# Optimization experiments

Hardware: AMD Instinct MI355X
Metric: run time of the kernel (lower is better)

## Reference

```python
import jax, jax.numpy as jnp
import numpy as np

N = 50000      # num nodes
E = 800000     # num edges
D = 64         # in_dim = hid_dim = out_dim
K = 8          # propagation hops (num_layers)
ALPHA = 0.6


def setup_inputs() -> dict:
    key = jax.random.key(0)
    ks = jax.random.split(key, 6)
    s = 1.0 / np.sqrt(D)
    return {
        "x": jax.random.normal(ks[0], (N, D), jnp.float32),
        "w_conv": jax.random.normal(ks[1], (D, D), jnp.float32) * s,
        "b_conv": jnp.zeros((D,), jnp.float32),
        "w1": jax.random.normal(ks[2], (D, D), jnp.float32) * s,
        "b1": jnp.zeros((D,), jnp.float32),
        "w2": jax.random.normal(ks[3], (D, D), jnp.float32) * s,
        "b2": jnp.zeros((D,), jnp.float32),
        "edge_index": jax.random.randint(ks[4], (2, E), 0, N, jnp.int64),
    }


def _gcn_norm(edge_index, num_nodes):
    # add self loops, symmetric normalization D^-1/2 (A+I) D^-1/2
    loop = jnp.arange(num_nodes, dtype=edge_index.dtype)
    src = jnp.concatenate([edge_index[0], loop])
    dst = jnp.concatenate([edge_index[1], loop])
    ones = jnp.ones(src.shape[0], jnp.float32)
    deg = jax.ops.segment_sum(ones, dst, num_segments=num_nodes)
    dinv = jnp.where(deg > 0, jax.lax.rsqrt(deg), 0.0)
    norm = dinv[src] * dinv[dst]  # [E+N]
    return src, dst, norm


def reference(x, w_conv, b_conv, w1, b1, w2, b2, edge_index):
    num_nodes = x.shape[0]
    src, dst, norm = _gcn_norm(edge_index, num_nodes)
    # SSGConv: h = alpha*x + (1-alpha)/K * sum_k A_hat^k x
    h = ALPHA * x
    xk = x
    coef = (1.0 - ALPHA) / K
    for _ in range(K):
        xk = jax.ops.segment_sum(norm[:, None] * xk[src], dst, num_segments=num_nodes)
        h = h + coef * xk
    h = h @ w_conv.T + b_conv        # SSGConv's internal Linear
    h = jax.nn.relu(h)               # F.relu(conv1(...))
    h = jax.nn.relu(h @ w1.T + b1)   # lin1 + relu (dropout p=0, eval)
    return h @ w2.T + b2             # lin2
```

## Files before the change

### kernel.cpp

```cpp
#include <hip/hip_runtime.h>

#define DD 64
#define ALPHA 0.6f
#define KHOPS 8
#define WP 72

typedef __attribute__((ext_vector_type(8))) short bf16x8;
typedef __attribute__((ext_vector_type(4))) float f32x4;

static __device__ __forceinline__ unsigned short f2bf(float f) {
    unsigned int u = __float_as_uint(f);
    unsigned int r = (u + 0x7FFFu + ((u >> 16) & 1u)) >> 16;
    return (unsigned short)r;
}
static __device__ __forceinline__ unsigned int pack2bf(float lo, float hi) {
    return (unsigned int)f2bf(lo) | ((unsigned int)f2bf(hi) << 16);
}

__global__ __launch_bounds__(256) void deg_count_kernel(const int* __restrict__ dst,
                                                        int* __restrict__ cnt, int e) {
    int i = blockIdx.x * blockDim.x + threadIdx.x;
    if (i < e) atomicAdd(&cnt[dst[i]], 1);
}

__global__ __launch_bounds__(256) void dinv_kernel(const int* __restrict__ cnt,
                                                   float2* __restrict__ dinvr, int n) {
    int i = blockIdx.x * blockDim.x + threadIdx.x;
    if (i < n) {
        float d = (float)(cnt[i] + 1);
        dinvr[i] = make_float2(rsqrtf(d), sqrtf(d));
    }
}

__global__ __launch_bounds__(256) void scan1_kernel(const int* __restrict__ cnt,
                                                    int* __restrict__ partials, int n) {
    int i = blockIdx.x * 256 + threadIdx.x;
    int v = (i < n) ? cnt[i] : 0;
    #pragma unroll
    for (int off = 1; off < 64; off <<= 1) v += __shfl_down(v, off, 64);
    __shared__ int ws[4];
    if ((threadIdx.x & 63) == 0) ws[threadIdx.x >> 6] = v;
    __syncthreads();
    if (threadIdx.x == 0) partials[blockIdx.x] = ws[0] + ws[1] + ws[2] + ws[3];
}

__global__ __launch_bounds__(1024) void scan2_kernel(int* __restrict__ partials, int nb) {
    __shared__ int s[1024];
    int t = threadIdx.x;
    int v = (t < nb) ? partials[t] : 0;
    s[t] = v;
    __syncthreads();
    for (int off = 1; off < 1024; off <<= 1) {
        int tmp = (t >= off) ? s[t - off] : 0;
        __syncthreads();
        s[t] += tmp;
        __syncthreads();
    }
    if (t < nb) partials[t] = s[t] - v;
}

__global__ __launch_bounds__(256) void scan3_kernel(const int* __restrict__ cnt,
                                                    const int* __restrict__ partials,
                                                    int* __restrict__ rowptr,
                                                    int* __restrict__ cursor, int n) {
    int t = threadIdx.x;
    int i = blockIdx.x * 256 + t;
    int v = (i < n) ? cnt[i] : 0;
    int lane = t & 63;
    int incl = v;
    #pragma unroll
    for (int off = 1; off < 64; off <<= 1) {
        int u = __shfl_up(incl, off, 64);
        if (lane >= off) incl += u;
    }
    __shared__ int wsum[4];
    if (lane == 63) wsum[t >> 6] = incl;
    __syncthreads();
    int woff = 0;
    for (int w = 0; w < (t >> 6); ++w) woff += wsum[w];
    int excl = incl - v + woff + partials[blockIdx.x];
    if (i < n) { rowptr[i] = excl; cursor[i] = excl; }
    if (i == n - 1) rowptr[n] = excl + v;
}

__global__ __launch_bounds__(256) void fill_kernel(const int* __restrict__ src,
                                                   const int* __restrict__ dst,
                                                   int* __restrict__ cursor,
                                                   int* __restrict__ esrc, int e) {
    int i = blockIdx.x * blockDim.x + threadIdx.x;
    if (i >= e) return;
    int s = src[i], d = dst[i];
    int pos = atomicAdd(&cursor[d], 1);
    __builtin_nontemporal_store(s, &esrc[pos]);
}

__global__ __launch_bounds__(256) void init_kernel(const float4* __restrict__ x,
                                                   const float2* __restrict__ dinvr,
                                                   float4* __restrict__ h,
                                                   ushort4* __restrict__ yb, int n4) {
    int i = blockIdx.x * blockDim.x + threadIdx.x;
    if (i >= n4) return;
    int row = i >> 4;
    float di = dinvr[row].x;
    float4 v = x[i];
    h[i] = make_float4(ALPHA * v.x, ALPHA * v.y, ALPHA * v.z, ALPHA * v.w);
    ushort4 b;
    b.x = f2bf(di * v.x); b.y = f2bf(di * v.y);
    b.z = f2bf(di * v.z); b.w = f2bf(di * v.w);
    yb[i] = b;
}

static __device__ __forceinline__ void add8(float* acc, uint4 v) {
    acc[0] += __uint_as_float(v.x << 16);
    acc[1] += __uint_as_float(v.x & 0xffff0000u);
    acc[2] += __uint_as_float(v.y << 16);
    acc[3] += __uint_as_float(v.y & 0xffff0000u);
    acc[4] += __uint_as_float(v.z << 16);
    acc[5] += __uint_as_float(v.z & 0xffff0000u);
    acc[6] += __uint_as_float(v.w << 16);
    acc[7] += __uint_as_float(v.w & 0xffff0000u);
}

template <int DO_H>
__global__ __launch_bounds__(256) void hop_kernel(const int* __restrict__ rowptr,
                                                  const int* __restrict__ esrc,
                                                  const float2* __restrict__ dinvr,
                                                  const unsigned short* __restrict__ yin,
                                                  unsigned short* __restrict__ yout,
                                                  float* __restrict__ h,
                                                  float coef, int n) {
    int wid = (blockIdx.x * blockDim.x + threadIdx.x) >> 6;
    if (wid >= n) return;
    int lane = threadIdx.x & 63;
    int g = lane >> 3;
    int s = lane & 7;
    int node = wid;

    int e0 = rowptr[node];
    int e1 = rowptr[node + 1];

    float acc[8] = {0.f, 0.f, 0.f, 0.f, 0.f, 0.f, 0.f, 0.f};
    float yprev[8];
    float2 dr;

    if (g == 0) {
        dr = dinvr[node];
        uint4 v = *(const uint4*)(yin + (size_t)node * 64 + s * 8);
        yprev[0] = __uint_as_float(v.x << 16);
        yprev[1] = __uint_as_float(v.x & 0xffff0000u);
        yprev[2] = __uint_as_float(v.y << 16);
        yprev[3] = __uint_as_float(v.y & 0xffff0000u);
        yprev[4] = __uint_as_float(v.z << 16);
        yprev[5] = __uint_as_float(v.z & 0xffff0000u);
        yprev[6] = __uint_as_float(v.w << 16);
        yprev[7] = __uint_as_float(v.w & 0xffff0000u);
        #pragma unroll
        for (int j = 0; j < 8; ++j) acc[j] = yprev[j];
    }

    int deg = e1 - e0;
    int niter = (deg + 7) >> 3;
    int i = 0;
    for (; i + 1 < niter; i += 2) {
        int eA = e0 + (i << 3) + g;
        int eB = eA + 8;
        int sA = esrc[eA];
        bool vB = eB < e1;
        int sB = esrc[vB ? eB : (e1 - 1)];
        uint4 va = *(const uint4*)(yin + (size_t)sA * 64 + s * 8);
        uint4 vb = *(const uint4*)(yin + (size_t)sB * 64 + s * 8);
        if (!vB) vb = make_uint4(0u, 0u, 0u, 0u);
        add8(acc, va);
        add8(acc, vb);
    }
    if (i < niter) {
        int eA = e0 + (i << 3) + g;
        bool vA = eA < e1;
        int sA = esrc[vA ? eA : (e1 - 1)];
        uint4 va = *(const uint4*)(yin + (size_t)sA * 64 + s * 8);
        if (!vA) va = make_uint4(0u, 0u, 0u, 0u);
        add8(acc, va);
    }

    #pragma unroll
    for (int off = 8; off < 64; off <<= 1) {
        #pragma unroll
        for (int j = 0; j < 8; ++j) acc[j] += __shfl_xor(acc[j], off, 64);
    }

    if (g == 0) {
        float di = dr.x;
        float d2 = di * di;
        uint4 o;
        o.x = pack2bf(d2 * acc[0], d2 * acc[1]);
        o.y = pack2bf(d2 * acc[2], d2 * acc[3]);
        o.z = pack2bf(d2 * acc[4], d2 * acc[5]);
        o.w = pack2bf(d2 * acc[6], d2 * acc[7]);
        *(uint4*)(yout + (size_t)node * 64 + s * 8) = o;
        if (DO_H) {
            float rd = dr.y;
            float* hp = h + (size_t)node * 64 + s * 8;
            float4 h0 = *(float4*)hp;
            float4 h1 = *(float4*)(hp + 4);
            h0.x += coef * (rd * yprev[0] + di * acc[0]);
            h0.y += coef * (rd * yprev[1] + di * acc[1]);
            h0.z += coef * (rd * yprev[2] + di * acc[2]);
            h0.w += coef * (rd * yprev[3] + di * acc[3]);
            h1.x += coef * (rd * yprev[4] + di * acc[4]);
            h1.y += coef * (rd * yprev[5] + di * acc[5]);
            h1.z += coef * (rd * yprev[6] + di * acc[6]);
            h1.w += coef * (rd * yprev[7] + di * acc[7]);
            *(float4*)hp = h0;
            *(float4*)(hp + 4) = h1;
        }
    }
}

__global__ __launch_bounds__(256) void mlp_mfma_kernel(const float* __restrict__ hin,
                                                       const float* __restrict__ wc,
                                                       const float* __restrict__ bc,
                                                       const float* __restrict__ w1,
                                                       const float* __restrict__ b1,
                                                       const float* __restrict__ w2,
                                                       const float* __restrict__ b2,
                                                       float* __restrict__ out, int n) {
    __shared__ unsigned short wlds[3][64][WP];
    __shared__ unsigned short xlds[64][WP];
    int t = threadIdx.x;

    const float* wm[3] = {wc, w1, w2};
    #pragma unroll
    for (int m = 0; m < 3; ++m) {
        const float4* w4 = (const float4*)wm[m];
        #pragma unroll
        for (int k = 0; k < 4; ++k) {
            int fid = t + k * 256;
            int j = fid >> 4, c4 = fid & 15;
            float4 v = w4[fid];
            *(uint2*)&wlds[m][j][c4 * 4] =
                make_uint2(pack2bf(v.x, v.y), pack2bf(v.z, v.w));
        }
    }

    int r0 = blockIdx.x * 64;
    const float4* h4 = (const float4*)hin;
    #pragma unroll
    for (int k = 0; k < 4; ++k) {
        int fid = t + k * 256;
        int r = fid >> 4, c4 = fid & 15;
        int gr = r0 + r;
        float4 v = (gr < n) ? h4[(size_t)gr * 16 + c4]
                            : make_float4(0.f, 0.f, 0.f, 0.f);
        *(uint2*)&xlds[r][c4 * 4] = make_uint2(pack2bf(v.x, v.y), pack2bf(v.z, v.w));
    }
    __syncthreads();

    int lane = t & 63;
    int wv = t >> 6;
    int rbase = wv * 16;
    int lr = lane & 15;
    int kg = lane >> 4;
    const float* bias[3] = {bc, b1, b2};

    #pragma unroll
    for (int m = 0; m < 3; ++m) {
        bf16x8 a0 = *(bf16x8*)&xlds[rbase + lr][kg * 8];
        bf16x8 a1 = *(bf16x8*)&xlds[rbase + lr][32 + kg * 8];
        #pragma unroll
        for (int ct = 0; ct < 4; ++ct) {
            bf16x8 bv0 = *(bf16x8*)&wlds[m][ct * 16 + lr][kg * 8];
            bf16x8 bv1 = *(bf16x8*)&wlds[m][ct * 16 + lr][32 + kg * 8];
            f32x4 acc = {0.f, 0.f, 0.f, 0.f};
            acc = __builtin_amdgcn_mfma_f32_16x16x32_bf16(a0, bv0, acc, 0, 0, 0);
            acc = __builtin_amdgcn_mfma_f32_16x16x32_bf16(a1, bv1, acc, 0, 0, 0);
            float bb = bias[m][ct * 16 + lr];
            if (m < 2) {
                #pragma unroll
                for (int rg = 0; rg < 4; ++rg) {
                    float v = fmaxf(acc[rg] + bb, 0.0f);
                    xlds[rbase + kg * 4 + rg][ct * 16 + lr] = f2bf(v);
                }
            } else {
                #pragma unroll
                for (int rg = 0; rg < 4; ++rg) {
                    int gr = r0 + rbase + kg * 4 + rg;
                    if (gr < n) out[(size_t)gr * 64 + ct * 16 + lr] = acc[rg] + bb;
                }
            }
        }
    }
}

extern "C" void kernel_launch(void* const* d_in, const int* in_sizes, int n_in,
                              void* d_out, int out_size, void* d_ws, size_t ws_size,
                              hipStream_t stream) {
    const float* x      = (const float*)d_in[0];
    const float* w_conv = (const float*)d_in[1];
    const float* b_conv = (const float*)d_in[2];
    const float* w1     = (const float*)d_in[3];
    const float* b1     = (const float*)d_in[4];
    const float* w2     = (const float*)d_in[5];
    const float* b2     = (const float*)d_in[6];
    const int*   ei     = (const int*)d_in[7];

    int n = in_sizes[0] / DD;
    int e = in_sizes[7] / 2;
    const int* src = ei;
    const int* dst = ei + e;

    char* wsb = (char*)d_ws;
    int*    cnt      = (int*)(wsb + 0);
    float2* dinvr    = (float2*)(wsb + 256 * 1024);
    int*    rowptr   = (int*)(wsb + 768 * 1024);
    int*    cursor   = (int*)(wsb + 1024 * 1024);
    int*    partials = (int*)(wsb + 1280 * 1024);
    int*    esrc     = (int*)(wsb + 1344 * 1024);
    unsigned short* yb0 = (unsigned short*)(wsb + 1344 * 1024 + (size_t)e * 4);
    unsigned short* yb1 = yb0 + (size_t)n * DD;
    float* h = (float*)d_out;

    const int B = 256;
    int n4 = n * (DD / 4);
    int nb = (n + 255) / 256;

    hipMemsetAsync(cnt, 0, (size_t)n * sizeof(int), stream);
    deg_count_kernel<<<(e + B - 1) / B, B, 0, stream>>>(dst, cnt, e);
    dinv_kernel<<<(n + B - 1) / B, B, 0, stream>>>(cnt, dinvr, n);
    scan1_kernel<<<nb, B, 0, stream>>>(cnt, partials, n);
    scan2_kernel<<<1, 1024, 0, stream>>>(partials, nb);
    scan3_kernel<<<nb, B, 0, stream>>>(cnt, partials, rowptr, cursor, n);
    fill_kernel<<<(e + B - 1) / B, B, 0, stream>>>(src, dst, cursor, esrc, e);

    init_kernel<<<(n4 + B - 1) / B, B, 0, stream>>>(
        (const float4*)x, dinvr, (float4*)h, (ushort4*)yb0, n4);

    float coef = (1.0f - ALPHA) / (float)KHOPS;
    int hblocks = (int)(((size_t)n * 64 + B - 1) / B);

    unsigned short* cur = yb0;
    unsigned short* nxt = yb1;
    for (int k = 1; k <= KHOPS; ++k) {
        if (k % 2 == 0)
            hop_kernel<1><<<hblocks, B, 0, stream>>>(rowptr, esrc, dinvr, cur, nxt, h,
                                                     coef, n);
        else
            hop_kernel<0><<<hblocks, B, 0, stream>>>(rowptr, esrc, dinvr, cur, nxt, h,
                                                     coef, n);
        unsigned short* tmp = cur; cur = nxt; nxt = tmp;
    }

    mlp_mfma_kernel<<<(n + 63) / 64, B, 0, stream>>>(h, w_conv, b_conv, w1, b1,
                                                     w2, b2, (float*)d_out, n);
}
```

Before: 305.6 us.

## Partition CSR fill by XCD destination range and unroll hop gather by four

```diff
diff --git a/kernel.cpp b/kernel.cpp
--- a/kernel.cpp
+++ b/kernel.cpp
@@ -83,15 +83,33 @@
     if (i == n - 1) rowptr[n] = excl + v;
 }
 
+#define FCHUNK 2048
 __global__ __launch_bounds__(256) void fill_kernel(const int* __restrict__ src,
                                                    const int* __restrict__ dst,
                                                    int* __restrict__ cursor,
-                                                   int* __restrict__ esrc, int e) {
-    int i = blockIdx.x * blockDim.x + threadIdx.x;
-    if (i >= e) return;
-    int s = src[i], d = dst[i];
-    int pos = atomicAdd(&cursor[d], 1);
-    __builtin_nontemporal_store(s, &esrc[pos]);
+                                                   int* __restrict__ esrc, int e, int n) {
+    int xcd = blockIdx.x & 7;
+    int chunk = blockIdx.x >> 3;
+    int lo = (int)(((long long)n * xcd) >> 3);
+    int hi = (int)(((long long)n * (xcd + 1)) >> 3);
+    int base = chunk * FCHUNK + threadIdx.x * 8;
+    if (base >= e) return;
+    int4 s0 = *(const int4*)(src + base);
+    int4 s1 = *(const int4*)(src + base + 4);
+    int4 d0 = *(const int4*)(dst + base);
+    int4 d1 = *(const int4*)(dst + base + 4);
+    int sv[8] = {s0.x, s0.y, s0.z, s0.w, s1.x, s1.y, s1.z, s1.w};
+    int dv[8] = {d0.x, d0.y, d0.z, d0.w, d1.x, d1.y, d1.z, d1.w};
+    #pragma unroll
+    for (int j = 0; j < 8; ++j) {
+        if (base + j < e) {
+            int d = dv[j];
+            if (d >= lo && d < hi) {
+                int pos = atomicAdd(&cursor[d], 1);
+                esrc[pos] = sv[j];
+            }
+        }
+    }
 }
 
 __global__ __launch_bounds__(256) void init_kernel(const float4* __restrict__ x,
@@ -160,26 +178,27 @@
 
     int deg = e1 - e0;
     int niter = (deg + 7) >> 3;
-    int i = 0;
-    for (; i + 1 < niter; i += 2) {
+    int clampe = e1 - 1;
+    for (int i = 0; i < niter; i += 4) {
         int eA = e0 + (i << 3) + g;
-        int eB = eA + 8;
-        int sA = esrc[eA];
-        bool vB = eB < e1;
-        int sB = esrc[vB ? eB : (e1 - 1)];
+        int eB = eA + 8, eC = eA + 16, eD = eA + 24;
+        bool vA = eA < e1, vB = eB < e1, vC = eC < e1, vD = eD < e1;
+        int sA = esrc[vA ? eA : clampe];
+        int sB = esrc[vB ? eB : clampe];
+        int sC = esrc[vC ? eC : clampe];
+        int sD = esrc[vD ? eD : clampe];
         uint4 va = *(const uint4*)(yin + (size_t)sA * 64 + s * 8);
         uint4 vb = *(const uint4*)(yin + (size_t)sB * 64 + s * 8);
+        uint4 vc = *(const uint4*)(yin + (size_t)sC * 64 + s * 8);
+        uint4 vd = *(const uint4*)(yin + (size_t)sD * 64 + s * 8);
+        if (!vA) va = make_uint4(0u, 0u, 0u, 0u);
         if (!vB) vb = make_uint4(0u, 0u, 0u, 0u);
+        if (!vC) vc = make_uint4(0u, 0u, 0u, 0u);
+        if (!vD) vd = make_uint4(0u, 0u, 0u, 0u);
         add8(acc, va);
         add8(acc, vb);
-    }
-    if (i < niter) {
-        int eA = e0 + (i << 3) + g;
-        bool vA = eA < e1;
-        int sA = esrc[vA ? eA : (e1 - 1)];
-        uint4 va = *(const uint4*)(yin + (size_t)sA * 64 + s * 8);
-        if (!vA) va = make_uint4(0u, 0u, 0u, 0u);
-        add8(acc, va);
+        add8(acc, vc);
+        add8(acc, vd);
     }
 
     #pragma unroll
@@ -329,7 +348,8 @@
     scan1_kernel<<<nb, B, 0, stream>>>(cnt, partials, n);
     scan2_kernel<<<1, 1024, 0, stream>>>(partials, nb);
     scan3_kernel<<<nb, B, 0, stream>>>(cnt, partials, rowptr, cursor, n);
-    fill_kernel<<<(e + B - 1) / B, B, 0, stream>>>(src, dst, cursor, esrc, e);
+    int nchunks = (e + FCHUNK - 1) / FCHUNK;
+    fill_kernel<<<nchunks * 8, B, 0, stream>>>(src, dst, cursor, esrc, e, n);
 
     init_kernel<<<(n4 + B - 1) / B, B, 0, stream>>>(
         (const float4*)x, dinvr, (float4*)h, (ushort4*)yb0, n4);
```

New measurement: 280.9 us. 8.1% less time.
